# Kernel optimization log

Measured on AMD Instinct MI355X. Metric: run time of the kernel, lower is better.

Reference implementation:

```python
import jax, jax.numpy as jnp
import numpy as np

NEG_INF = -1e30


def _cc_attention(q, k, v):
    # q,k: [B,H,W,c], v: [B,H,W,C]
    B, H, W, _ = q.shape
    # vertical scores over column: [B,H,W,H], diag (h==g) masked out
    sv = jnp.einsum('bhwc,bgwc->bhwg', q, k)
    eye = jnp.eye(H, dtype=bool)[:, None, :]  # [H,1,H]
    sv = jnp.where(eye, NEG_INF, sv)
    # horizontal scores over row: [B,H,W,W]
    sh = jnp.einsum('bhwc,bhuc->bhwu', q, k)
    a = jax.nn.softmax(jnp.concatenate([sv, sh], axis=-1), axis=-1)
    av, ah = a[..., :H], a[..., H:H + W]
    yv = jnp.einsum('bhwg,bgwc->bhwc', av, v)
    yh = jnp.einsum('bhwu,bhuc->bhwc', ah, v)
    return yv + yh


def setup_inputs() -> dict:
    key = jax.random.key(0)
    ks = jax.random.split(key, 7)
    B, H, W, C = 8, 96, 96, 512
    c = C // 8
    s = lambda n: 1.0 / np.sqrt(n)
    return {
        'x': jax.random.normal(ks[0], (B, H, W, C), jnp.float32),
        'Wq': jax.random.normal(ks[1], (C, c), jnp.float32) * s(C),
        'bq': jnp.zeros((c,), jnp.float32),
        'Wk': jax.random.normal(ks[2], (C, c), jnp.float32) * s(C),
        'bk': jnp.zeros((c,), jnp.float32),
        'Wv': jax.random.normal(ks[3], (C, C), jnp.float32) * s(C),
        'bv': jnp.zeros((C,), jnp.float32),
        'gamma': jnp.float32(0.5),
    }


def reference(x, Wq, bq, Wk, bk, Wv, bv, gamma):
    # 1x1 convs == per-pixel matmul
    q = jnp.einsum('bhwc,cd->bhwd', x, Wq) + bq
    k = jnp.einsum('bhwc,cd->bhwd', x, Wk) + bk
    v = jnp.einsum('bhwc,cd->bhwd', x, Wv) + bv
    y = _cc_attention(q, k, v) * gamma
    return y + x
```

## Files before the change

### kernel.cpp

```cpp
#include <hip/hip_runtime.h>
#include <hip/hip_bf16.h>


#define NPIX 73728
#define HH 96
#define WW 96
#define CC 512
#define CQ 64
#define PA 384

typedef __attribute__((ext_vector_type(8))) short bf16x8;
typedef __attribute__((ext_vector_type(4))) float f32x4;

__device__ __forceinline__ void async16(const void* g, void* l) {
    __builtin_amdgcn_global_load_lds(
        (const __attribute__((address_space(1))) unsigned int*)g,
        (__attribute__((address_space(3))) unsigned int*)l,
        16, 0, 0);
}

__global__ __launch_bounds__(256) void conv_x(
    const float* __restrict__ x, short* __restrict__ xb)
{
    size_t i8 = ((size_t)blockIdx.x * 256 + threadIdx.x) * 8;
    float4 a = *reinterpret_cast<const float4*>(x + i8);
    float4 b = *reinterpret_cast<const float4*>(x + i8 + 4);
    union { __hip_bfloat16 h[8]; uint4 u; } pk;
    pk.h[0] = __float2bfloat16(a.x); pk.h[1] = __float2bfloat16(a.y);
    pk.h[2] = __float2bfloat16(a.z); pk.h[3] = __float2bfloat16(a.w);
    pk.h[4] = __float2bfloat16(b.x); pk.h[5] = __float2bfloat16(b.y);
    pk.h[6] = __float2bfloat16(b.z); pk.h[7] = __float2bfloat16(b.w);
    *reinterpret_cast<uint4*>(xb + i8) = pk.u;
}

__global__ __launch_bounds__(256) void conv_w(
    const float* __restrict__ W, short* __restrict__ dst, int J)
{
    int idx = blockIdx.x * 256 + threadIdx.x;
    int lane = idx & 63;
    int blk = idx >> 6;
    int ntiles = J >> 4;
    int ntile = blk % ntiles;
    int kb32 = blk / ntiles;
    int krow = kb32 * 32 + (lane >> 4) * 8;
    int col = ntile * 16 + (lane & 15);
    union { __hip_bfloat16 h[8]; uint4 u; } pk;
    #pragma unroll
    for (int j = 0; j < 8; ++j)
        pk.h[j] = __float2bfloat16(W[(size_t)(krow + j) * J + col]);
    *reinterpret_cast<uint4*>(dst + (size_t)idx * 8) = pk.u;
}

template <int BN>
__global__ __launch_bounds__(256) void mfma_proj(
    const short* __restrict__ Xb,
    const short* __restrict__ Wf,
    const float* __restrict__ bias,
    short* __restrict__ out,
    int J)
{
    __shared__ __align__(16) short Albuf[128 * 32];
    const int tid = threadIdx.x;
    const int lane = tid & 63;
    const int w = tid >> 6;
    const int mBase = blockIdx.x * 128;
    const int nBase = blockIdx.y * BN;

    constexpr int MT = (BN == 128) ? 4 : 2;
    constexpr int NT = 4;
    const int wr = (BN == 128) ? (w >> 1) : w;
    const int wc = (BN == 128) ? (w & 1) : 0;
    const int tbase = wr * MT;
    const int nTile0 = (nBase >> 4) + wc * 4;
    const int ntilesJ = J >> 4;

    f32x4 acc[MT][NT];
    #pragma unroll
    for (int i = 0; i < MT; ++i)
        #pragma unroll
        for (int j = 0; j < NT; ++j) {
            f32x4 z = {0.f, 0.f, 0.f, 0.f};
            acc[i][j] = z;
        }

    const int arow0 = lane & 15;
    const int acol0 = (lane >> 4) * 8;

    for (int kb = 0; kb < 16; ++kb) {
        #pragma unroll
        for (int s = 0; s < 2; ++s) {
            int t = w * 2 + s;
            const short* g = Xb + (size_t)(mBase + t * 16 + arow0) * 512 + kb * 32 + acol0;
            async16(g, &Albuf[t * 512]);
        }
        __syncthreads();

        bf16x8 bf[NT];
        #pragma unroll
        for (int jn = 0; jn < NT; ++jn)
            bf[jn] = *reinterpret_cast<const bf16x8*>(
                Wf + ((size_t)(kb * ntilesJ + nTile0 + jn) * 64 + lane) * 8);
        bf16x8 af[MT];
        #pragma unroll
        for (int i = 0; i < MT; ++i)
            af[i] = *reinterpret_cast<const bf16x8*>(&Albuf[(tbase + i) * 512 + lane * 8]);
        #pragma unroll
        for (int i = 0; i < MT; ++i)
            #pragma unroll
            for (int jn = 0; jn < NT; ++jn)
                acc[i][jn] = __builtin_amdgcn_mfma_f32_16x16x32_bf16(
                    af[i], bf[jn], acc[i][jn], 0, 0, 0);
        __syncthreads();
    }

    const int lrow = (lane >> 4) * 4, lcol = lane & 15;
    #pragma unroll
    for (int jn = 0; jn < NT; ++jn) {
        int col = nBase + wc * 64 + jn * 16 + lcol;
        float bc = bias[col];
        #pragma unroll
        for (int i = 0; i < MT; ++i) {
            int row = mBase + wr * (MT * 16) + i * 16 + lrow;
            #pragma unroll
            for (int r = 0; r < 4; ++r) {
                __hip_bfloat16 hb = __float2bfloat16(acc[i][jn][r] + bc);
                out[(size_t)(row + r) * J + col] = *reinterpret_cast<short*>(&hb);
            }
        }
    }
}

__global__ __launch_bounds__(256) void cc_scores(
    const short* __restrict__ Q,
    const short* __restrict__ K,
    float* __restrict__ S)
{
    const int tid = threadIdx.x;
    const int lane = tid & 63;
    const int wv = tid >> 6;
    const int wr = wv >> 1, wc = wv & 1;
    const bool vert = (blockIdx.y == 0);
    const int b = blockIdx.x / 96;
    const int line = blockIdx.x % 96;

    size_t base;
    int rowStride;
    if (vert) { base = (size_t)b * 9216 + line;       rowStride = 96; }
    else      { base = ((size_t)b * 96 + line) * 96;  rowStride = 1;  }

    const int cl = lane & 15;
    const int q8 = (lane >> 4) * 8;

    f32x4 acc[3][3];
    #pragma unroll
    for (int i = 0; i < 3; ++i)
        #pragma unroll
        for (int j = 0; j < 3; ++j) {
            f32x4 z = {0.f, 0.f, 0.f, 0.f};
            acc[i][j] = z;
        }

    #pragma unroll
    for (int kb = 0; kb < 2; ++kb) {
        bf16x8 af[3], bf[3];
        #pragma unroll
        for (int mt = 0; mt < 3; ++mt) {
            size_t n = base + (size_t)(wr * 48 + mt * 16 + cl) * rowStride;
            af[mt] = *reinterpret_cast<const bf16x8*>(Q + n * 64 + kb * 32 + q8);
        }
        #pragma unroll
        for (int nt = 0; nt < 3; ++nt) {
            size_t n = base + (size_t)(wc * 48 + nt * 16 + cl) * rowStride;
            bf[nt] = *reinterpret_cast<const bf16x8*>(K + n * 64 + kb * 32 + q8);
        }
        #pragma unroll
        for (int mt = 0; mt < 3; ++mt)
            #pragma unroll
            for (int nt = 0; nt < 3; ++nt)
                acc[mt][nt] = __builtin_amdgcn_mfma_f32_16x16x32_bf16(
                    af[mt], bf[nt], acc[mt][nt], 0, 0, 0);
    }

    const int lrow = (lane >> 4) * 4;
    const int dirOff = vert ? 0 : 96;
    #pragma unroll
    for (int mt = 0; mt < 3; ++mt) {
        #pragma unroll
        for (int r = 0; r < 4; ++r) {
            int i = wr * 48 + mt * 16 + lrow + r;
            size_t n = base + (size_t)i * rowStride;
            float* srow = S + n * 192 + dirOff;
            #pragma unroll
            for (int nt = 0; nt < 3; ++nt) {
                int j = wc * 48 + nt * 16 + cl;
                srow[j] = (vert && i == j) ? -1e30f : acc[mt][nt][r];
            }
        }
    }
}

__global__ __launch_bounds__(256) void cc_softmax(float* __restrict__ S)
{
    const int tid = threadIdx.x;
    const int lane = tid & 63;
    const size_t n = (size_t)blockIdx.x * 4 + (tid >> 6);
    float* row = S + n * 192;
    float s0 = row[lane], s1 = row[lane + 64], s2 = row[lane + 128];
    float m = fmaxf(s0, fmaxf(s1, s2));
    #pragma unroll
    for (int off = 32; off >= 1; off >>= 1) m = fmaxf(m, __shfl_xor(m, off, 64));
    float e0 = expf(s0 - m), e1 = expf(s1 - m), e2 = expf(s2 - m);
    float sum = e0 + e1 + e2;
    #pragma unroll
    for (int off = 32; off >= 1; off >>= 1) sum += __shfl_xor(sum, off, 64);
    float inv = 1.0f / sum;
    __hip_bfloat16 p0 = __float2bfloat16(e0 * inv);
    __hip_bfloat16 p1 = __float2bfloat16(e1 * inv);
    __hip_bfloat16 p2 = __float2bfloat16(e2 * inv);
    short* av = reinterpret_cast<short*>(row);
    short* ah = av + 96;
    av[lane] = *reinterpret_cast<short*>(&p0);
    if (lane < 32) av[64 + lane] = *reinterpret_cast<short*>(&p1);
    else           ah[lane - 32] = *reinterpret_cast<short*>(&p1);
    ah[32 + lane] = *reinterpret_cast<short*>(&p2);
}

__global__ __launch_bounds__(256) void cc_aggr_v(
    const short* __restrict__ A,
    const short* __restrict__ V,
    short* __restrict__ Yv)
{
    __shared__ __align__(16) short Vs[96 * 128];
    const int tid = threadIdx.x;
    const int lane = tid & 63;
    const int wv = tid >> 6;
    const int b = blockIdx.x / 96;
    const int w = blockIdx.x % 96;
    const int cBase = blockIdx.y * 128;
    const size_t colBase = (size_t)b * 9216 + w;

    #pragma unroll
    for (int s = 0; s < 6; ++s) {
        int c0 = (s * 4 + wv) * 64;
        int chunk = c0 + lane;
        int g = chunk >> 4;
        int cc = (chunk & 15) * 8;
        async16(V + (colBase + (size_t)g * 96) * 512 + cBase + cc,
                &Vs[(size_t)c0 * 8]);
    }
    __syncthreads();

    const int wr = wv >> 1, wc = wv & 1;
    const int cl = lane & 15, q = lane >> 4;

    f32x4 acc[3][4];
    #pragma unroll
    for (int i = 0; i < 3; ++i)
        #pragma unroll
        for (int j = 0; j < 4; ++j) {
            f32x4 z = {0.f, 0.f, 0.f, 0.f};
            acc[i][j] = z;
        }

    for (int kb = 0; kb < 3; ++kb) {
        bf16x8 af[3];
        #pragma unroll
        for (int mt = 0; mt < 3; ++mt) {
            size_t n = colBase + (size_t)(wr * 48 + mt * 16 + cl) * 96;
            af[mt] = *reinterpret_cast<const bf16x8*>(A + n * PA + kb * 32 + q * 8);
        }
        #pragma unroll
        for (int nt = 0; nt < 4; ++nt) {
            int col = wc * 64 + nt * 16 + cl;
            bf16x8 bv;
            #pragma unroll
            for (int j = 0; j < 8; ++j)
                bv[j] = Vs[(kb * 32 + q * 8 + j) * 128 + col];
            #pragma unroll
            for (int mt = 0; mt < 3; ++mt)
                acc[mt][nt] = __builtin_amdgcn_mfma_f32_16x16x32_bf16(
                    af[mt], bv, acc[mt][nt], 0, 0, 0);
        }
    }

    const int lrow = q * 4;
    #pragma unroll
    for (int mt = 0; mt < 3; ++mt) {
        #pragma unroll
        for (int r = 0; r < 4; ++r) {
            size_t n = colBase + (size_t)(wr * 48 + mt * 16 + lrow + r) * 96;
            #pragma unroll
            for (int nt = 0; nt < 4; ++nt) {
                int c = cBase + wc * 64 + nt * 16 + cl;
                __hip_bfloat16 hb = __float2bfloat16(acc[mt][nt][r]);
                Yv[n * 512 + c] = *reinterpret_cast<short*>(&hb);
            }
        }
    }
}

__global__ __launch_bounds__(256) void cc_aggr_h_final(
    const short* __restrict__ A,
    const short* __restrict__ V,
    const __hip_bfloat16* __restrict__ Yv,
    const float* __restrict__ X,
    const float* __restrict__ gamma_p,
    float* __restrict__ out)
{
    __shared__ __align__(16) short Vs[96 * 128];
    const int tid = threadIdx.x;
    const int lane = tid & 63;
    const int wv = tid >> 6;
    const int b = blockIdx.x / 96;
    const int h = blockIdx.x % 96;
    const int cBase = blockIdx.y * 128;
    const size_t rowBase = (size_t)(b * 96 + h) * 96;

    #pragma unroll
    for (int s = 0; s < 6; ++s) {
        int c0 = (s * 4 + wv) * 64;
        int chunk = c0 + lane;
        int u = chunk >> 4;
        int cc = (chunk & 15) * 8;
        async16(V + (rowBase + u) * 512 + cBase + cc,
                &Vs[(size_t)c0 * 8]);
    }
    __syncthreads();

    const int wr = wv >> 1, wc = wv & 1;
    const int cl = lane & 15, q = lane >> 4;

    f32x4 acc[3][4];
    #pragma unroll
    for (int i = 0; i < 3; ++i)
        #pragma unroll
        for (int j = 0; j < 4; ++j) {
            f32x4 z = {0.f, 0.f, 0.f, 0.f};
            acc[i][j] = z;
        }

    for (int kb = 0; kb < 3; ++kb) {
        bf16x8 af[3];
        #pragma unroll
        for (int mt = 0; mt < 3; ++mt) {
            size_t n = rowBase + (size_t)(wr * 48 + mt * 16 + cl);
            af[mt] = *reinterpret_cast<const bf16x8*>(A + n * PA + 96 + kb * 32 + q * 8);
        }
        #pragma unroll
        for (int nt = 0; nt < 4; ++nt) {
            int col = wc * 64 + nt * 16 + cl;
            bf16x8 bv;
            #pragma unroll
            for (int j = 0; j < 8; ++j)
                bv[j] = Vs[(kb * 32 + q * 8 + j) * 128 + col];
            #pragma unroll
            for (int mt = 0; mt < 3; ++mt)
                acc[mt][nt] = __builtin_amdgcn_mfma_f32_16x16x32_bf16(
                    af[mt], bv, acc[mt][nt], 0, 0, 0);
        }
    }

    const float gm = gamma_p[0];
    const int lrow = q * 4;
    #pragma unroll
    for (int mt = 0; mt < 3; ++mt) {
        #pragma unroll
        for (int r = 0; r < 4; ++r) {
            size_t n = rowBase + (size_t)(wr * 48 + mt * 16 + lrow + r);
            size_t rowOff = n * 512;
            #pragma unroll
            for (int nt = 0; nt < 4; ++nt) {
                int c = cBase + wc * 64 + nt * 16 + cl;
                size_t off = rowOff + c;
                out[off] = (acc[mt][nt][r] + __bfloat162float(Yv[off])) * gm + X[off];
            }
        }
    }
}

extern "C" void kernel_launch(void* const* d_in, const int* in_sizes, int n_in,
                              void* d_out, int out_size, void* d_ws, size_t ws_size,
                              hipStream_t stream) {
    const float* x     = (const float*)d_in[0];
    const float* Wq    = (const float*)d_in[1];
    const float* bq    = (const float*)d_in[2];
    const float* Wk    = (const float*)d_in[3];
    const float* bk    = (const float*)d_in[4];
    const float* Wv    = (const float*)d_in[5];
    const float* bv    = (const float*)d_in[6];
    const float* gamma = (const float*)d_in[7];
    float* out = (float*)d_out;

    short* xb  = (short*)d_ws;
    short* Wqf = xb + (size_t)NPIX * 512;
    short* Wkf = Wqf + 512 * 64;
    short* Wvf = Wkf + 512 * 64;
    short* q   = Wvf + 512 * 512;
    short* k   = q + (size_t)NPIX * CQ;
    short* v   = k + (size_t)NPIX * CQ;
    float* S   = (float*)(v + (size_t)NPIX * CC);
    __hip_bfloat16* yv = (__hip_bfloat16*)xb;

    conv_x<<<NPIX * 512 / 8 / 256, 256, 0, stream>>>(x, xb);
    conv_w<<<16, 256, 0, stream>>>(Wq, Wqf, 64);
    conv_w<<<16, 256, 0, stream>>>(Wk, Wkf, 64);
    conv_w<<<128, 256, 0, stream>>>(Wv, Wvf, 512);

    mfma_proj<64><<<dim3(NPIX / 128, 1), 256, 0, stream>>>(xb, Wqf, bq, q, CQ);
    mfma_proj<64><<<dim3(NPIX / 128, 1), 256, 0, stream>>>(xb, Wkf, bk, k, CQ);
    mfma_proj<128><<<dim3(NPIX / 128, 4), 256, 0, stream>>>(xb, Wvf, bv, v, CC);

    cc_scores<<<dim3(8 * 96, 2), 256, 0, stream>>>(q, k, S);
    cc_softmax<<<NPIX / 4, 256, 0, stream>>>(S);

    cc_aggr_v<<<dim3(8 * 96, 4), 256, 0, stream>>>((const short*)S, v, (short*)yv);
    cc_aggr_h_final<<<dim3(8 * 96, 4), 256, 0, stream>>>(
        (const short*)S, v, yv, x, gamma, out);
}
```

Measured before the change: 628.2 us.

## Emit channel-major transposed V layouts so aggregation reads vectorised B fragments

Replaces the single row-major V projection with two projection kernels that write V channel-major, one ordered along rows and one along columns. The aggregation kernels can then load MFMA B operands as 16-byte vectors straight from global memory instead of staging V in LDS and gathering scalars. The cost is running the V projection GEMM twice, which doubles that work and the V workspace, and the column-ordered variant gathers X with strided row access. Grid indexing is also flattened so the four channel blocks of one line are adjacent.

After: 660.4 us. +5.1%, slower.

```diff
diff --git a/kernel.cpp b/kernel.cpp
--- a/kernel.cpp
+++ b/kernel.cpp
@@ -17,6 +17,11 @@
         (const __attribute__((address_space(1))) unsigned int*)g,
         (__attribute__((address_space(3))) unsigned int*)l,
         16, 0, 0);
+}
+
+__device__ __forceinline__ short bf16s(float f) {
+    __hip_bfloat16 h = __float2bfloat16(f);
+    return *reinterpret_cast<short*>(&h);
 }
 
 __global__ __launch_bounds__(256) void conv_x(
@@ -123,9 +128,163 @@
             int row = mBase + wr * (MT * 16) + i * 16 + lrow;
             #pragma unroll
             for (int r = 0; r < 4; ++r) {
-                __hip_bfloat16 hb = __float2bfloat16(acc[i][jn][r] + bc);
-                out[(size_t)(row + r) * J + col] = *reinterpret_cast<short*>(&hb);
+                out[(size_t)(row + r) * J + col] = bf16s(acc[i][jn][r] + bc);
             }
+        }
+    }
+}
+
+__global__ __launch_bounds__(256) void proj_v_th(
+    const short* __restrict__ Xb,
+    const short* __restrict__ Wf,
+    const float* __restrict__ bias,
+    short* __restrict__ vth)
+{
+    __shared__ __align__(16) short Albuf[128 * 32];
+    const int tid = threadIdx.x;
+    const int lane = tid & 63;
+    const int w = tid >> 6;
+    const int bid = blockIdx.x;
+    const int mBase = (bid >> 2) * 128;
+    const int nBase = (bid & 3) * 128;
+
+    const int wr = w >> 1, wc = w & 1;
+    const int nTile0 = (nBase >> 4) + wc * 4;
+
+    f32x4 acc[4][4];
+    #pragma unroll
+    for (int i = 0; i < 4; ++i)
+        #pragma unroll
+        for (int j = 0; j < 4; ++j) {
+            f32x4 z = {0.f, 0.f, 0.f, 0.f};
+            acc[i][j] = z;
+        }
+
+    const int arow0 = lane & 15;
+    const int acol0 = (lane >> 4) * 8;
+
+    for (int kb = 0; kb < 16; ++kb) {
+        #pragma unroll
+        for (int s = 0; s < 2; ++s) {
+            int t = w * 2 + s;
+            const short* g = Xb + (size_t)(mBase + t * 16 + arow0) * 512 + kb * 32 + acol0;
+            async16(g, &Albuf[t * 512]);
+        }
+        __syncthreads();
+
+        bf16x8 bf[4];
+        #pragma unroll
+        for (int jn = 0; jn < 4; ++jn)
+            bf[jn] = *reinterpret_cast<const bf16x8*>(
+                Wf + ((size_t)(kb * 32 + nTile0 + jn) * 64 + lane) * 8);
+        bf16x8 af[4];
+        #pragma unroll
+        for (int i = 0; i < 4; ++i)
+            af[i] = *reinterpret_cast<const bf16x8*>(&Albuf[(wr * 4 + i) * 512 + lane * 8]);
+        #pragma unroll
+        for (int i = 0; i < 4; ++i)
+            #pragma unroll
+            for (int jn = 0; jn < 4; ++jn)
+                acc[i][jn] = __builtin_amdgcn_mfma_f32_16x16x32_bf16(
+                    af[i], bf[jn], acc[i][jn], 0, 0, 0);
+        __syncthreads();
+    }
+
+    const int lrow = (lane >> 4) * 4, lcol = lane & 15;
+    #pragma unroll
+    for (int jn = 0; jn < 4; ++jn) {
+        int col = nBase + wc * 64 + jn * 16 + lcol;
+        float bc = bias[col];
+        #pragma unroll
+        for (int i = 0; i < 4; ++i) {
+            int row = mBase + wr * 64 + i * 16 + lrow;
+            short4 st;
+            st.x = bf16s(acc[i][jn][0] + bc);
+            st.y = bf16s(acc[i][jn][1] + bc);
+            st.z = bf16s(acc[i][jn][2] + bc);
+            st.w = bf16s(acc[i][jn][3] + bc);
+            *reinterpret_cast<short4*>(vth + (size_t)col * NPIX + row) = st;
+        }
+    }
+}
+
+__global__ __launch_bounds__(256) void proj_v_tv(
+    const short* __restrict__ Xb,
+    const short* __restrict__ Wf,
+    const float* __restrict__ bias,
+    short* __restrict__ vtv)
+{
+    __shared__ __align__(16) short Albuf[96 * 32];
+    const int tid = threadIdx.x;
+    const int lane = tid & 63;
+    const int wv = tid >> 6;
+    const int bid = blockIdx.x;
+    const int pair = bid >> 2;
+    const int nBase = (bid & 3) * 128;
+    const int b = pair / 96;
+    const int w = pair - b * 96;
+    const size_t colPix = (size_t)b * 9216 + w;
+    const size_t wBase = (size_t)b * 9216 + (size_t)w * 96;
+
+    const int wr = wv >> 1, wc = wv & 1;
+    const int nTile0 = (nBase >> 4) + wc * 4;
+
+    f32x4 acc[3][4];
+    #pragma unroll
+    for (int i = 0; i < 3; ++i)
+        #pragma unroll
+        for (int j = 0; j < 4; ++j) {
+            f32x4 z = {0.f, 0.f, 0.f, 0.f};
+            acc[i][j] = z;
+        }
+
+    const int arow0 = lane & 15;
+    const int acol0 = (lane >> 4) * 8;
+
+    for (int kb = 0; kb < 16; ++kb) {
+        #pragma unroll
+        for (int s = 0; s < 2; ++s) {
+            int t = s * 4 + wv;
+            if (t < 6) {
+                const short* g = Xb + (colPix + (size_t)(t * 16 + arow0) * 96) * 512
+                                    + kb * 32 + acol0;
+                async16(g, &Albuf[t * 512]);
+            }
+        }
+        __syncthreads();
+
+        bf16x8 bf[4];
+        #pragma unroll
+        for (int jn = 0; jn < 4; ++jn)
+            bf[jn] = *reinterpret_cast<const bf16x8*>(
+                Wf + ((size_t)(kb * 32 + nTile0 + jn) * 64 + lane) * 8);
+        bf16x8 af[3];
+        #pragma unroll
+        for (int i = 0; i < 3; ++i)
+            af[i] = *reinterpret_cast<const bf16x8*>(&Albuf[(wr * 3 + i) * 512 + lane * 8]);
+        #pragma unroll
+        for (int i = 0; i < 3; ++i)
+            #pragma unroll
+            for (int jn = 0; jn < 4; ++jn)
+                acc[i][jn] = __builtin_amdgcn_mfma_f32_16x16x32_bf16(
+                    af[i], bf[jn], acc[i][jn], 0, 0, 0);
+        __syncthreads();
+    }
+
+    const int lrow = (lane >> 4) * 4, lcol = lane & 15;
+    #pragma unroll
+    for (int jn = 0; jn < 4; ++jn) {
+        int col = nBase + wc * 64 + jn * 16 + lcol;
+        float bc = bias[col];
+        #pragma unroll
+        for (int i = 0; i < 3; ++i) {
+            int h = wr * 48 + i * 16 + lrow;
+            short4 st;
+            st.x = bf16s(acc[i][jn][0] + bc);
+            st.y = bf16s(acc[i][jn][1] + bc);
+            st.z = bf16s(acc[i][jn][2] + bc);
+            st.w = bf16s(acc[i][jn][3] + bc);
+            *reinterpret_cast<short4*>(vtv + (size_t)col * NPIX + wBase + h) = st;
         }
     }
 }
@@ -214,41 +373,32 @@
     #pragma unroll
     for (int off = 32; off >= 1; off >>= 1) sum += __shfl_xor(sum, off, 64);
     float inv = 1.0f / sum;
-    __hip_bfloat16 p0 = __float2bfloat16(e0 * inv);
-    __hip_bfloat16 p1 = __float2bfloat16(e1 * inv);
-    __hip_bfloat16 p2 = __float2bfloat16(e2 * inv);
+    short p0 = bf16s(e0 * inv);
+    short p1 = bf16s(e1 * inv);
+    short p2 = bf16s(e2 * inv);
     short* av = reinterpret_cast<short*>(row);
     short* ah = av + 96;
-    av[lane] = *reinterpret_cast<short*>(&p0);
-    if (lane < 32) av[64 + lane] = *reinterpret_cast<short*>(&p1);
-    else           ah[lane - 32] = *reinterpret_cast<short*>(&p1);
-    ah[32 + lane] = *reinterpret_cast<short*>(&p2);
+    av[lane] = p0;
+    if (lane < 32) av[64 + lane] = p1;
+    else           ah[lane - 32] = p1;
+    ah[32 + lane] = p2;
 }
 
 __global__ __launch_bounds__(256) void cc_aggr_v(
     const short* __restrict__ A,
-    const short* __restrict__ V,
+    const short* __restrict__ vtv,
     short* __restrict__ Yv)
 {
-    __shared__ __align__(16) short Vs[96 * 128];
     const int tid = threadIdx.x;
     const int lane = tid & 63;
     const int wv = tid >> 6;
-    const int b = blockIdx.x / 96;
-    const int w = blockIdx.x % 96;
-    const int cBase = blockIdx.y * 128;
-    const size_t colBase = (size_t)b * 9216 + w;
-
-    #pragma unroll
-    for (int s = 0; s < 6; ++s) {
-        int c0 = (s * 4 + wv) * 64;
-        int chunk = c0 + lane;
-        int g = chunk >> 4;
-        int cc = (chunk & 15) * 8;
-        async16(V + (colBase + (size_t)g * 96) * 512 + cBase + cc,
-                &Vs[(size_t)c0 * 8]);
-    }
-    __syncthreads();
+    const int bid = blockIdx.x;
+    const int pair = bid >> 2;
+    const int cBase = (bid & 3) * 128;
+    const int b = pair / 96;
+    const int w = pair - b * 96;
+    const size_t pixBase = (size_t)b * 9216 + w;
+    const size_t wBase = (size_t)b * 9216 + (size_t)w * 96;
 
     const int wr = wv >> 1, wc = wv & 1;
     const int cl = lane & 15, q = lane >> 4;
@@ -262,20 +412,19 @@
             acc[i][j] = z;
         }
 
+    #pragma unroll
     for (int kb = 0; kb < 3; ++kb) {
         bf16x8 af[3];
         #pragma unroll
         for (int mt = 0; mt < 3; ++mt) {
-            size_t n = colBase + (size_t)(wr * 48 + mt * 16 + cl) * 96;
+            size_t n = pixBase + (size_t)(wr * 48 + mt * 16 + cl) * 96;
             af[mt] = *reinterpret_cast<const bf16x8*>(A + n * PA + kb * 32 + q * 8);
         }
         #pragma unroll
         for (int nt = 0; nt < 4; ++nt) {
-            int col = wc * 64 + nt * 16 + cl;
-            bf16x8 bv;
-            #pragma unroll
-            for (int j = 0; j < 8; ++j)
-                bv[j] = Vs[(kb * 32 + q * 8 + j) * 128 + col];
+            int col = cBase + wc * 64 + nt * 16 + cl;
+            bf16x8 bv = *reinterpret_cast<const bf16x8*>(
+                vtv + (size_t)col * NPIX + wBase + kb * 32 + q * 8);
             #pragma unroll
             for (int mt = 0; mt < 3; ++mt)
                 acc[mt][nt] = __builtin_amdgcn_mfma_f32_16x16x32_bf16(
@@ -288,12 +437,11 @@
     for (int mt = 0; mt < 3; ++mt) {
         #pragma unroll
         for (int r = 0; r < 4; ++r) {
-            size_t n = colBase + (size_t)(wr * 48 + mt * 16 + lrow + r) * 96;
+            size_t n = pixBase + (size_t)(wr * 48 + mt * 16 + lrow + r) * 96;
             #pragma unroll
             for (int nt = 0; nt < 4; ++nt) {
                 int c = cBase + wc * 64 + nt * 16 + cl;
-                __hip_bfloat16 hb = __float2bfloat16(acc[mt][nt][r]);
-                Yv[n * 512 + c] = *reinterpret_cast<short*>(&hb);
+                Yv[n * 512 + c] = bf16s(acc[mt][nt][r]);
             }
         }
     }
@@ -301,31 +449,19 @@
 
 __global__ __launch_bounds__(256) void cc_aggr_h_final(
     const short* __restrict__ A,
-    const short* __restrict__ V,
+    const short* __restrict__ vth,
     const __hip_bfloat16* __restrict__ Yv,
     const float* __restrict__ X,
     const float* __restrict__ gamma_p,
     float* __restrict__ out)
 {
-    __shared__ __align__(16) short Vs[96 * 128];
     const int tid = threadIdx.x;
     const int lane = tid & 63;
     const int wv = tid >> 6;
-    const int b = blockIdx.x / 96;
-    const int h = blockIdx.x % 96;
-    const int cBase = blockIdx.y * 128;
-    const size_t rowBase = (size_t)(b * 96 + h) * 96;
-
-    #pragma unroll
-    for (int s = 0; s < 6; ++s) {
-        int c0 = (s * 4 + wv) * 64;
-        int chunk = c0 + lane;
-        int u = chunk >> 4;
-        int cc = (chunk & 15) * 8;
-        async16(V + (rowBase + u) * 512 + cBase + cc,
-                &Vs[(size_t)c0 * 8]);
-    }
-    __syncthreads();
+    const int bid = blockIdx.x;
+    const int pair = bid >> 2;
+    const int cBase = (bid & 3) * 128;
+    const size_t rowBase = (size_t)pair * 96;
 
     const int wr = wv >> 1, wc = wv & 1;
     const int cl = lane & 15, q = lane >> 4;
@@ -339,6 +475,7 @@
             acc[i][j] = z;
         }
 
+    #pragma unroll
     for (int kb = 0; kb < 3; ++kb) {
         bf16x8 af[3];
         #pragma unroll
@@ -348,11 +485,9 @@
         }
         #pragma unroll
         for (int nt = 0; nt < 4; ++nt) {
-            int col = wc * 64 + nt * 16 + cl;
-            bf16x8 bv;
-            #pragma unroll
-            for (int j = 0; j < 8; ++j)
-                bv[j] = Vs[(kb * 32 + q * 8 + j) * 128 + col];
+            int col = cBase + wc * 64 + nt * 16 + cl;
+            bf16x8 bv = *reinterpret_cast<const bf16x8*>(
+                vth + (size_t)col * NPIX + rowBase + kb * 32 + q * 8);
             #pragma unroll
             for (int mt = 0; mt < 3; ++mt)
                 acc[mt][nt] = __builtin_amdgcn_mfma_f32_16x16x32_bf16(
@@ -366,12 +501,10 @@
     for (int mt = 0; mt < 3; ++mt) {
         #pragma unroll
         for (int r = 0; r < 4; ++r) {
-            size_t n = rowBase + (size_t)(wr * 48 + mt * 16 + lrow + r);
-            size_t rowOff = n * 512;
+            size_t rowOff = (rowBase + (size_t)(wr * 48 + mt * 16 + lrow + r)) * 512;
             #pragma unroll
             for (int nt = 0; nt < 4; ++nt) {
-                int c = cBase + wc * 64 + nt * 16 + cl;
-                size_t off = rowOff + c;
+                size_t off = rowOff + cBase + wc * 64 + nt * 16 + cl;
                 out[off] = (acc[mt][nt][r] + __bfloat162float(Yv[off])) * gm + X[off];
             }
         }
@@ -397,9 +530,10 @@
     short* Wvf = Wkf + 512 * 64;
     short* q   = Wvf + 512 * 512;
     short* k   = q + (size_t)NPIX * CQ;
-    short* v   = k + (size_t)NPIX * CQ;
-    float* S   = (float*)(v + (size_t)NPIX * CC);
-    __hip_bfloat16* yv = (__hip_bfloat16*)xb;
+    short* vth = k + (size_t)NPIX * CQ;
+    short* vtv = vth + (size_t)NPIX * CC;
+    float* S   = (float*)(vtv + (size_t)NPIX * CC);
+    short* yv  = xb;
 
     conv_x<<<NPIX * 512 / 8 / 256, 256, 0, stream>>>(x, xb);
     conv_w<<<16, 256, 0, stream>>>(Wq, Wqf, 64);
@@ -408,12 +542,13 @@
 
     mfma_proj<64><<<dim3(NPIX / 128, 1), 256, 0, stream>>>(xb, Wqf, bq, q, CQ);
     mfma_proj<64><<<dim3(NPIX / 128, 1), 256, 0, stream>>>(xb, Wkf, bk, k, CQ);
-    mfma_proj<128><<<dim3(NPIX / 128, 4), 256, 0, stream>>>(xb, Wvf, bv, v, CC);
+    proj_v_th<<<(NPIX / 128) * 4, 256, 0, stream>>>(xb, Wvf, bv, vth);
+    proj_v_tv<<<768 * 4, 256, 0, stream>>>(xb, Wvf, bv, vtv);
 
     cc_scores<<<dim3(8 * 96, 2), 256, 0, stream>>>(q, k, S);
     cc_softmax<<<NPIX / 4, 256, 0, stream>>>(S);
 
-    cc_aggr_v<<<dim3(8 * 96, 4), 256, 0, stream>>>((const short*)S, v, (short*)yv);
-    cc_aggr_h_final<<<dim3(8 * 96, 4), 256, 0, stream>>>(
-        (const short*)S, v, yv, x, gamma, out);
-}
+    cc_aggr_v<<<768 * 4, 256, 0, stream>>>((const short*)S, vtv, yv);
+    cc_aggr_h_final<<<768 * 4, 256, 0, stream>>>(
+        (const short*)S, vth, (const __hip_bfloat16*)yv, x, gamma, out);
+}
```
